# Optimization experiments

Hardware: AMD Instinct MI355X
Metric: run time of the kernel (lower is better)

## Reference

```python
import jax, jax.numpy as jnp
import numpy as np

REDUCE_RATIO = 0.9

def reference(x, starts):
    # x: [B, T, C] float; starts: [B] int, start of the cropped window per sample.
    B, T, C = x.shape
    L = int(np.ceil(REDUCE_RATIO * T))  # target_len (static)
    # np.interp query points: linspace(0, L, num=T) against xp = arange(L).
    q = jnp.linspace(0.0, float(L), T, dtype=x.dtype)          # [T]
    t = jnp.clip(q, 0.0, float(L - 1))                          # np.interp clamps to edges
    lo = jnp.clip(jnp.floor(t), 0.0, float(L - 2)).astype(jnp.int32)  # [T]
    w = (t - lo.astype(x.dtype))[None, :, None]                 # [1, T, 1] interp weight
    # Absolute gather indices into the original series: start + local index.
    idx_lo = starts[:, None].astype(jnp.int32) + lo[None, :]    # [B, T]
    v_lo = jnp.take_along_axis(x, idx_lo[:, :, None], axis=1)       # [B, T, C]
    v_hi = jnp.take_along_axis(x, (idx_lo + 1)[:, :, None], axis=1)  # [B, T, C]
    return v_lo * (1.0 - w) + v_hi * w

def setup_inputs() -> dict:
    key = jax.random.key(0)
    k1, k2 = jax.random.split(key)
    B, T, C = 64, 4096, 128
    L = int(np.ceil(REDUCE_RATIO * T))
    x = jax.random.normal(k1, (B, T, C), dtype=jnp.float32)
    starts = jax.random.randint(k2, (B,), 0, T - L, dtype=jnp.int32)
    return {"x": x, "starts": starts}
```

## Files before the change

### kernel.cpp

```cpp
#include <hip/hip_runtime.h>


constexpr int B_ = 64;
constexpr int T_ = 4096;
constexpr int C_ = 128;
constexpr int L_ = 3687;
constexpr int C4 = C_ / 4;

__global__ __launch_bounds__(256)
void WindowSlice_kernel(const float4* __restrict__ x,
                        const int*    __restrict__ starts,
                        float4*       __restrict__ out) {
    const int tid = blockIdx.x * 256 + threadIdx.x;
    const int row = tid >> 5;
    const int c4  = tid & 31;
    const int b   = row >> 12;
    const int i   = row & (T_ - 1);

    const double step = (double)L_ / (double)(T_ - 1);
    double t = (double)i * step;
    if (t > (double)(L_ - 1)) t = (double)(L_ - 1);
    int lo = (int)t;
    if (lo > L_ - 2) lo = L_ - 2;
    const float w = (float)(t - (double)lo);

    const int start = starts[b];
    const long long base = ((long long)b * T_ + start + lo) * C4 + c4;

    const float4 vlo = x[base];
    const float4 vhi = x[base + C4];

    float4 o;
    o.x = fmaf(w, vhi.x - vlo.x, vlo.x);
    o.y = fmaf(w, vhi.y - vlo.y, vlo.y);
    o.z = fmaf(w, vhi.z - vlo.z, vlo.z);
    o.w = fmaf(w, vhi.w - vlo.w, vlo.w);

    out[(long long)row * C4 + c4] = o;
}

extern "C" void kernel_launch(void* const* d_in, const int* in_sizes, int n_in,
                              void* d_out, int out_size, void* d_ws, size_t ws_size,
                              hipStream_t stream) {
    const float4* x      = (const float4*)d_in[0];
    const int*    starts = (const int*)d_in[1];
    float4*       out    = (float4*)d_out;

    const int total_f4 = B_ * T_ * C4;
    const int blocks   = total_f4 / 256;
    WindowSlice_kernel<<<blocks, 256, 0, stream>>>(x, starts, out);
}
```

Baseline: 224.7 us.

## Remap blocks per XCD, double work per thread, use float interpolation math

Reorders block indices so each XCD gets a contiguous range of rows. Adjacent rows share source lines, so this aims to improve L2 reuse of the overlapping lo/hi reads. Each thread now handles two float4 columns, halving the thread count, and the interpolation position is computed in float instead of double to avoid slow FP64 ops. Float math may change lo/w slightly near integer boundaries compared with the reference.

Result: no change. 228.7 us (+1.7%).

```diff
diff --git a/kernel.cpp b/kernel.cpp
--- a/kernel.cpp
+++ b/kernel.cpp
@@ -3,40 +3,50 @@
 
 constexpr int B_ = 64;
 constexpr int T_ = 4096;
-constexpr int C_ = 128;
 constexpr int L_ = 3687;
-constexpr int C4 = C_ / 4;
+constexpr int C4 = 32;
+constexpr int NBLK = (B_ * T_ * (C4 / 2)) / 256;
+constexpr int NXCD = 8;
+constexpr int BLK_PER_XCD = NBLK / NXCD;
 
 __global__ __launch_bounds__(256)
 void WindowSlice_kernel(const float4* __restrict__ x,
                         const int*    __restrict__ starts,
                         float4*       __restrict__ out) {
-    const int tid = blockIdx.x * 256 + threadIdx.x;
-    const int row = tid >> 5;
-    const int c4  = tid & 31;
+    const int lb  = (blockIdx.x & (NXCD - 1)) * BLK_PER_XCD + (blockIdx.x >> 3);
+    const int wid = lb * 256 + threadIdx.x;
+    const int row = wid >> 4;
+    const int c4  = wid & 15;
     const int b   = row >> 12;
     const int i   = row & (T_ - 1);
 
-    const double step = (double)L_ / (double)(T_ - 1);
-    double t = (double)i * step;
-    if (t > (double)(L_ - 1)) t = (double)(L_ - 1);
+    const float step = (float)L_ / (float)(T_ - 1);
+    float t = fminf((float)i * step, (float)(L_ - 1));
     int lo = (int)t;
-    if (lo > L_ - 2) lo = L_ - 2;
-    const float w = (float)(t - (double)lo);
+    lo = min(lo, L_ - 2);
+    const float w = t - (float)lo;
 
     const int start = starts[b];
     const long long base = ((long long)b * T_ + start + lo) * C4 + c4;
 
-    const float4 vlo = x[base];
-    const float4 vhi = x[base + C4];
+    const float4 a0 = x[base];
+    const float4 b0 = x[base + C4];
+    const float4 a1 = x[base + 16];
+    const float4 b1 = x[base + C4 + 16];
 
-    float4 o;
-    o.x = fmaf(w, vhi.x - vlo.x, vlo.x);
-    o.y = fmaf(w, vhi.y - vlo.y, vlo.y);
-    o.z = fmaf(w, vhi.z - vlo.z, vlo.z);
-    o.w = fmaf(w, vhi.w - vlo.w, vlo.w);
+    float4 o0, o1;
+    o0.x = fmaf(w, b0.x - a0.x, a0.x);
+    o0.y = fmaf(w, b0.y - a0.y, a0.y);
+    o0.z = fmaf(w, b0.z - a0.z, a0.z);
+    o0.w = fmaf(w, b0.w - a0.w, a0.w);
+    o1.x = fmaf(w, b1.x - a1.x, a1.x);
+    o1.y = fmaf(w, b1.y - a1.y, a1.y);
+    o1.z = fmaf(w, b1.z - a1.z, a1.z);
+    o1.w = fmaf(w, b1.w - a1.w, a1.w);
 
-    out[(long long)row * C4 + c4] = o;
+    const long long obase = (long long)row * C4 + c4;
+    out[obase]      = o0;
+    out[obase + 16] = o1;
 }
 
 extern "C" void kernel_launch(void* const* d_in, const int* in_sizes, int n_in,
@@ -46,7 +56,5 @@
     const int*    starts = (const int*)d_in[1];
     float4*       out    = (float4*)d_out;
 
-    const int total_f4 = B_ * T_ * C4;
-    const int blocks   = total_f4 / 256;
-    WindowSlice_kernel<<<blocks, 256, 0, stream>>>(x, starts, out);
+    WindowSlice_kernel<<<NBLK, 256, 0, stream>>>(x, starts, out);
 }
```
